# Kernel optimization log

Hardware: AMD Instinct MI355X
Metric: run time of the kernel (lower is better)

## Reference

```python
import jax, jax.numpy as jnp
import numpy as np

NUM_HEADS = 16
HEAD_DIM = 64
ROPE_BASE = 10000.0


def apply_rope(x):
    # x: [b, s, n_h, h_d]; pairwise rotation as in torchtune RotaryPositionalEmbeddings
    b, s, nh, hd = x.shape
    inv_freq = 1.0 / (ROPE_BASE ** (jnp.arange(0, hd, 2, dtype=jnp.float32) / hd))  # [hd/2]
    angles = jnp.arange(s, dtype=jnp.float32)[:, None] * inv_freq[None, :]          # [s, hd/2]
    cos = jnp.cos(angles)[None, :, None, :]  # [1, s, 1, hd/2]
    sin = jnp.sin(angles)[None, :, None, :]
    xp = x.reshape(b, s, nh, hd // 2, 2)
    x1, x2 = xp[..., 0], xp[..., 1]
    rot = jnp.stack([x1 * cos - x2 * sin, x1 * sin + x2 * cos], axis=-1)
    return rot.reshape(b, s, nh, hd)


def setup_inputs() -> dict:
    key = jax.random.key(0)
    k1, k2 = jax.random.split(key)
    B, S, D = 64, 200, 1024
    x = jax.random.normal(k1, (B, S, D), dtype=jnp.float32)
    # causal mask, realistic for a decoder; True = attend
    mask = jnp.broadcast_to(jnp.tril(jnp.ones((S, S), dtype=bool)), (B, S, S))
    W_qkv = jax.random.normal(k2, (3 * D, D), dtype=jnp.float32) * (1.0 / np.sqrt(D))
    b_qkv = jnp.zeros((3 * D,), dtype=jnp.float32)
    return {"x": x, "mask": mask, "W_qkv": W_qkv, "b_qkv": b_qkv}


def reference(x, mask, W_qkv, b_qkv):
    B, S, D = x.shape
    H, hd = NUM_HEADS, HEAD_DIM
    qkv = x @ W_qkv.T + b_qkv                      # [B, S, 3D]
    qkv = qkv.reshape(B, S, H, 3 * hd)
    q, k, v = jnp.split(qkv, 3, axis=-1)           # each [B, S, H, hd]
    q = apply_rope(q)
    k = apply_rope(k)
    q = q.transpose(0, 2, 1, 3)                    # [B, H, S, hd]
    k = k.transpose(0, 2, 1, 3)
    v = v.transpose(0, 2, 1, 3)
    logits = jnp.einsum("bhqd,bhkd->bhqk", q, k) / jnp.sqrt(jnp.float32(hd))
    logits = jnp.where(mask[:, None, :, :], logits, -jnp.inf)
    attn = jax.nn.softmax(logits, axis=-1)
    out = jnp.einsum("bhqk,bhkd->bhqd", attn, v)   # [B, H, S, hd]
    return out.transpose(0, 2, 1, 3).reshape(B, S, H * hd)
```

## Files before the change

### kernel.cpp

```cpp
#include <hip/hip_runtime.h>
#include <hip/hip_bf16.h>

#define BB 64
#define SS 200
#define DD 1024
#define HH 16
#define HD 64
#define N3 3072
#define MM (BB*SS)
#define KK DD
#define SPV 216

using half8 = __attribute__((ext_vector_type(8))) _Float16;
using f32x4 = __attribute__((ext_vector_type(4))) float;

__device__ __forceinline__ void gload16(const void* g, void* l) {
    __builtin_amdgcn_global_load_lds(
        (const __attribute__((address_space(1))) void*)g,
        (__attribute__((address_space(3))) void*)l, 16, 0, 0);
}

__global__ __launch_bounds__(256) void f32_to_f16_kernel(const float* __restrict__ in,
                                                         _Float16* __restrict__ out, int n8) {
    int i = blockIdx.x * 256 + threadIdx.x;
    int stride = gridDim.x * 256;
    for (; i < n8; i += stride) {
        float4 a = ((const float4*)in)[i * 2];
        float4 b = ((const float4*)in)[i * 2 + 1];
        half8 h;
        h[0] = (_Float16)a.x; h[1] = (_Float16)a.y; h[2] = (_Float16)a.z; h[3] = (_Float16)a.w;
        h[4] = (_Float16)b.x; h[5] = (_Float16)b.y; h[6] = (_Float16)b.z; h[7] = (_Float16)b.w;
        ((half8*)out)[i] = h;
    }
}

__global__ __launch_bounds__(256) void rope_table_kernel(float* __restrict__ rope) {
    int t = blockIdx.x * 256 + threadIdx.x;
    if (t >= SS * 32) return;
    int s = t >> 5, i = t & 31;
    float inv = powf(10000.0f, -(float)(2 * i) / 64.0f);
    float ang = (float)s * inv;
    rope[t * 2 + 0] = cosf(ang);
    rope[t * 2 + 1] = sinf(ang);
}

__device__ __forceinline__ void gemm_step(const _Float16* Asb, const _Float16* Bsb,
                                          int arow, int brow, int kq,
                                          f32x4 (&acc)[4][4]) {
    half8 af[4], bf[4];
    #pragma unroll
    for (int mi = 0; mi < 4; ++mi) {
        int r = arow + mi * 16;
        af[mi] = *(const half8*)&Asb[r * 32 + ((kq ^ ((r >> 1) & 3)) << 3)];
    }
    #pragma unroll
    for (int ni = 0; ni < 4; ++ni) {
        int r = brow + ni * 16;
        bf[ni] = *(const half8*)&Bsb[r * 32 + ((kq ^ ((r >> 1) & 3)) << 3)];
    }
    __builtin_amdgcn_s_setprio(1);
    #pragma unroll
    for (int mi = 0; mi < 4; ++mi)
        #pragma unroll
        for (int ni = 0; ni < 4; ++ni)
            acc[mi][ni] = __builtin_amdgcn_mfma_f32_16x16x32_f16(af[mi], bf[ni], acc[mi][ni], 0, 0, 0);
    __builtin_amdgcn_s_setprio(0);
}

__global__ __launch_bounds__(256) void qkv_gemm_f16_kernel(
    const _Float16* __restrict__ Xh, const _Float16* __restrict__ Wh,
    const float* __restrict__ bias, const float* __restrict__ rope,
    _Float16* __restrict__ qo, _Float16* __restrict__ ko, _Float16* __restrict__ vt)
{
    __shared__ _Float16 As[2][128 * 32];
    __shared__ _Float16 Bs[2][128 * 32];

    const int t = threadIdx.x;
    const int w = t >> 6, lane = t & 63;
    const int wm = w >> 1, wn = w & 1;
    const int m0 = blockIdx.y * 128, n0 = blockIdx.x * 128;

    f32x4 acc[4][4];
    #pragma unroll
    for (int i = 0; i < 4; ++i)
        #pragma unroll
        for (int j = 0; j < 4; ++j) acc[i][j] = (f32x4)0.f;

    int srow[2], scol[2], sdst[2];
    #pragma unroll
    for (int c = 0; c < 2; ++c) {
        int slot = c * 256 + t;
        int r = slot >> 2, sl = slot & 3;
        srow[c] = r;
        scol[c] = (sl ^ ((r >> 1) & 3)) << 3;
        sdst[c] = (c * 256 + w * 64) * 8;
    }
    const int arow = wm * 64 + (lane & 15);
    const int brow = wn * 64 + (lane & 15);
    const int kq = lane >> 4;

    const _Float16* Xb = Xh + (size_t)m0 * KK;
    const _Float16* Wb = Wh + (size_t)n0 * KK;

    #pragma unroll
    for (int c = 0; c < 2; ++c) {
        gload16(Xb + (size_t)srow[c] * KK + scol[c], &As[0][sdst[c]]);
        gload16(Wb + (size_t)srow[c] * KK + scol[c], &Bs[0][sdst[c]]);
    }
    asm volatile("s_waitcnt vmcnt(0)" ::: "memory");
    __builtin_amdgcn_s_barrier();

    for (int kt = 0; kt < KK; kt += 64) {
        #pragma unroll
        for (int c = 0; c < 2; ++c) {
            gload16(Xb + (size_t)srow[c] * KK + kt + 32 + scol[c], &As[1][sdst[c]]);
            gload16(Wb + (size_t)srow[c] * KK + kt + 32 + scol[c], &Bs[1][sdst[c]]);
        }
        gemm_step(As[0], Bs[0], arow, brow, kq, acc);
        asm volatile("s_waitcnt vmcnt(0)" ::: "memory");
        __builtin_amdgcn_s_barrier();
        if (kt + 64 < KK) {
            #pragma unroll
            for (int c = 0; c < 2; ++c) {
                gload16(Xb + (size_t)srow[c] * KK + kt + 64 + scol[c], &As[0][sdst[c]]);
                gload16(Wb + (size_t)srow[c] * KK + kt + 64 + scol[c], &Bs[0][sdst[c]]);
            }
        }
        gemm_step(As[1], Bs[1], arow, brow, kq, acc);
        asm volatile("s_waitcnt vmcnt(0)" ::: "memory");
        __builtin_amdgcn_s_barrier();
    }

    #pragma unroll
    for (int ni = 0; ni < 4; ++ni) {
        int n = n0 + wn * 64 + ni * 16 + (lane & 15);
        float bv = bias[n];
        int h = n / 192;
        int rr = n - h * 192;
        int which = rr >> 6;
        int j = rr & 63;
        int jp = j >> 1;
        #pragma unroll
        for (int mi = 0; mi < 4; ++mi) {
            #pragma unroll
            for (int reg = 0; reg < 4; ++reg) {
                int m = m0 + wm * 64 + mi * 16 + (lane >> 4) * 4 + reg;
                int b_ = m / SS, s_ = m - b_ * SS;
                float v = acc[mi][ni][reg] + bv;
                float p = __shfl_xor(v, 1);
                size_t bh = (size_t)b_ * HH + h;
                if (which == 2) {
                    vt[(bh * HD + j) * SPV + s_] = (_Float16)v;
                } else {
                    float2 cs = *(const float2*)&rope[(s_ * 32 + jp) * 2];
                    float o = (j & 1) ? fmaf(p, cs.y, v * cs.x) : fmaf(v, cs.x, -p * cs.y);
                    if (which == 0)
                        qo[(bh * SS + s_) * HD + j] = (_Float16)(o * 0.125f);
                    else
                        ko[(bh * SS + s_) * HD + j] = (_Float16)o;
                }
            }
        }
    }
}

__global__ __launch_bounds__(256) void attn_mfma_kernel(
    const _Float16* __restrict__ q, const _Float16* __restrict__ k,
    const _Float16* __restrict__ vt, float* __restrict__ out)
{
    __shared__ _Float16 Klds[256 * 64];
    __shared__ _Float16 VTlds[64 * SPV];
    __shared__ _Float16 Plds[4][32 * 64];

    const int bh = blockIdx.x;
    const int b_ = bh >> 4, h = bh & 15;
    const int t = threadIdx.x;
    const int w = t >> 6, lane = t & 63;
    const int l15 = lane & 15, l4 = lane >> 4;

    const _Float16* kbase = k + (size_t)bh * SS * HD;
    const _Float16* vtbase = vt + (size_t)bh * HD * SPV;
    const _Float16* qbase = q + (size_t)bh * SS * HD;

    for (int c = t; c < 256 * 8; c += 256) {
        int row = c >> 3, g = c & 7;
        int rowc = row < SS ? row : (SS - 1);
        float4 val = *(const float4*)(kbase + rowc * HD + g * 8);
        *(float4*)&Klds[row * 64 + ((g ^ (row & 7)) * 8)] = val;
    }
    for (int c = t; c < 64 * 27; c += 256) {
        int row = c / 27, g = c - row * 27;
        *(float4*)&VTlds[row * SPV + g * 8] = *(const float4*)(vtbase + row * SPV + g * 8);
    }
    __syncthreads();

    const int qts[2] = { (w == 3) ? 6 : w, 5 - w };
    const int nqt = (w == 3) ? 1 : 2;

    for (int qi = 0; qi < nqt; ++qi) {
        const int qt = qts[qi];
        const int q0 = qt * 32;
        const int nkt = (q0 + 95) >> 6;

        half8 qf[2][2];
        #pragma unroll
        for (int mt = 0; mt < 2; ++mt)
            #pragma unroll
            for (int ks = 0; ks < 2; ++ks)
                qf[mt][ks] = *(const half8*)(qbase + (size_t)(q0 + mt * 16 + l15) * HD + ks * 32 + l4 * 8);

        float mrow[2][4], lsum[2][4];
        f32x4 oacc[2][4];
        #pragma unroll
        for (int mt = 0; mt < 2; ++mt) {
            #pragma unroll
            for (int r = 0; r < 4; ++r) { mrow[mt][r] = -1e30f; lsum[mt][r] = 0.f; }
            #pragma unroll
            for (int nt = 0; nt < 4; ++nt) oacc[mt][nt] = (f32x4)0.f;
        }

        for (int ki = 0; ki < nkt; ++ki) {
            const int k0 = ki * 64;
            const bool lastk = (ki == nkt - 1);

            half8 kf[4][2];
            #pragma unroll
            for (int nt = 0; nt < 4; ++nt)
                #pragma unroll
                for (int ks = 0; ks < 2; ++ks) {
                    int row = k0 + nt * 16 + l15;
                    int g = l4 + ks * 4;
                    kf[nt][ks] = *(const half8*)&Klds[row * 64 + ((g ^ (row & 7)) * 8)];
                }
            f32x4 s[2][4];
            __builtin_amdgcn_s_setprio(1);
            #pragma unroll
            for (int mt = 0; mt < 2; ++mt)
                #pragma unroll
                for (int nt = 0; nt < 4; ++nt) {
                    f32x4 a = (f32x4)0.f;
                    a = __builtin_amdgcn_mfma_f32_16x16x32_f16(qf[mt][0], kf[nt][0], a, 0, 0, 0);
                    a = __builtin_amdgcn_mfma_f32_16x16x32_f16(qf[mt][1], kf[nt][1], a, 0, 0, 0);
                    s[mt][nt] = a;
                }
            __builtin_amdgcn_s_setprio(0);

            if (lastk) {
                #pragma unroll
                for (int mt = 0; mt < 2; ++mt)
                    #pragma unroll
                    for (int nt = 0; nt < 4; ++nt)
                        #pragma unroll
                        for (int r = 0; r < 4; ++r) {
                            int qq = q0 + mt * 16 + l4 * 4 + r;
                            int kk2 = k0 + nt * 16 + l15;
                            if (kk2 > qq || kk2 >= SS) s[mt][nt][r] = -1e30f;
                        }
            }

            #pragma unroll
            for (int mt = 0; mt < 2; ++mt) {
                float tmax[4];
                int ok = 1;
                #pragma unroll
                for (int r = 0; r < 4; ++r) {
                    float tm = fmaxf(fmaxf(s[mt][0][r], s[mt][1][r]),
                                     fmaxf(s[mt][2][r], s[mt][3][r]));
                    #pragma unroll
                    for (int off = 8; off > 0; off >>= 1)
                        tm = fmaxf(tm, __shfl_xor(tm, off));
                    tmax[r] = tm;
                    ok &= (tm <= mrow[mt][r] + 4.0f) ? 1 : 0;
                }
                if (__all(ok)) {
                    #pragma unroll
                    for (int r = 0; r < 4; ++r) {
                        float mo = mrow[mt][r];
                        float ps = 0.f;
                        #pragma unroll
                        for (int nt = 0; nt < 4; ++nt) {
                            float p = __expf(s[mt][nt][r] - mo);
                            s[mt][nt][r] = p;
                            ps += p;
                        }
                        lsum[mt][r] += ps;
                    }
                } else {
                    #pragma unroll
                    for (int r = 0; r < 4; ++r) {
                        float mo = mrow[mt][r];
                        float mn = fmaxf(mo, tmax[r]);
                        float sc = __expf(mo - mn);
                        mrow[mt][r] = mn;
                        float ps = 0.f;
                        #pragma unroll
                        for (int nt = 0; nt < 4; ++nt) {
                            float p = __expf(s[mt][nt][r] - mn);
                            s[mt][nt][r] = p;
                            ps += p;
                        }
                        lsum[mt][r] = lsum[mt][r] * sc + ps;
                        #pragma unroll
                        for (int nt = 0; nt < 4; ++nt)
                            oacc[mt][nt][r] *= sc;
                    }
                }
            }

            #pragma unroll
            for (int mt = 0; mt < 2; ++mt)
                #pragma unroll
                for (int nt = 0; nt < 4; ++nt)
                    #pragma unroll
                    for (int r = 0; r < 4; ++r) {
                        int row = mt * 16 + l4 * 4 + r;
                        int col = nt * 16 + l15;
                        Plds[w][row * 64 + (((col >> 3) ^ (row & 7)) * 8) + (col & 7)] =
                            (_Float16)s[mt][nt][r];
                    }

            half8 pa[2][2], vb[4][2];
            #pragma unroll
            for (int mt = 0; mt < 2; ++mt)
                #pragma unroll
                for (int ksl = 0; ksl < 2; ++ksl) {
                    int row = mt * 16 + l15;
                    pa[mt][ksl] = *(const half8*)&Plds[w][row * 64 + (((ksl * 4 + l4) ^ (row & 7)) * 8)];
                }
            #pragma unroll
            for (int nt = 0; nt < 4; ++nt)
                #pragma unroll
                for (int ksl = 0; ksl < 2; ++ksl) {
                    int koff = k0 + ksl * 32 + l4 * 8;
                    koff = (koff > SPV - 8) ? (SPV - 8) : koff;
                    vb[nt][ksl] = *(const half8*)&VTlds[(nt * 16 + l15) * SPV + koff];
                }
            __builtin_amdgcn_s_setprio(1);
            #pragma unroll
            for (int mt = 0; mt < 2; ++mt)
                #pragma unroll
                for (int nt = 0; nt < 4; ++nt) {
                    oacc[mt][nt] = __builtin_amdgcn_mfma_f32_16x16x32_f16(pa[mt][0], vb[nt][0], oacc[mt][nt], 0, 0, 0);
                    oacc[mt][nt] = __builtin_amdgcn_mfma_f32_16x16x32_f16(pa[mt][1], vb[nt][1], oacc[mt][nt], 0, 0, 0);
                }
            __builtin_amdgcn_s_setprio(0);
        }

        #pragma unroll
        for (int mt = 0; mt < 2; ++mt) {
            #pragma unroll
            for (int r = 0; r < 4; ++r) {
                float l = lsum[mt][r];
                #pragma unroll
                for (int off = 8; off > 0; off >>= 1)
                    l += __shfl_xor(l, off);
                int s_ = q0 + mt * 16 + l4 * 4 + r;
                if (s_ < SS) {
                    float rinv = 1.0f / l;
                    #pragma unroll
                    for (int nt = 0; nt < 4; ++nt)
                        out[((size_t)b_ * SS + s_) * DD + h * HD + nt * 16 + l15] = oacc[mt][nt][r] * rinv;
                }
            }
        }
    }
}

extern "C" void kernel_launch(void* const* d_in, const int* in_sizes, int n_in,
                              void* d_out, int out_size, void* d_ws, size_t ws_size,
                              hipStream_t stream) {
    const float* x    = (const float*)d_in[0];
    const float* W    = (const float*)d_in[2];
    const float* bias = (const float*)d_in[3];
    float* out = (float*)d_out;

    char* ws = (char*)d_ws;
    float*    rope = (float*)ws;
    _Float16* Xh   = (_Float16*)(ws + 65536);
    _Float16* Wh   = (_Float16*)(ws + 65536 + 26214400ull);
    _Float16* Qh   = (_Float16*)(ws + 65536 + 26214400ull + 6291456ull);
    _Float16* Kh   = Qh + (size_t)BB * HH * SS * HD;
    _Float16* VTh  = Kh + (size_t)BB * HH * SS * HD;

    f32_to_f16_kernel<<<2048, 256, 0, stream>>>(x, Xh, MM * KK / 8);
    f32_to_f16_kernel<<<1024, 256, 0, stream>>>(W, Wh, N3 * KK / 8);
    rope_table_kernel<<<(SS * 32 + 255) / 256, 256, 0, stream>>>(rope);
    qkv_gemm_f16_kernel<<<dim3(N3 / 128, MM / 128), dim3(256), 0, stream>>>(Xh, Wh, bias, rope, Qh, Kh, VTh);
    attn_mfma_kernel<<<BB * HH, 256, 0, stream>>>(Qh, Kh, VTh, out);
}
```

Baseline: 356.0 us.

## Deepen QKV GEMM global-to-LDS pipeline to four stages with partial vmcnt waits

```diff
diff --git a/kernel.cpp b/kernel.cpp
--- a/kernel.cpp
+++ b/kernel.cpp
@@ -72,8 +72,8 @@
     const float* __restrict__ bias, const float* __restrict__ rope,
     _Float16* __restrict__ qo, _Float16* __restrict__ ko, _Float16* __restrict__ vt)
 {
-    __shared__ _Float16 As[2][128 * 32];
-    __shared__ _Float16 Bs[2][128 * 32];
+    __shared__ _Float16 As[4][128 * 32];
+    __shared__ _Float16 Bs[4][128 * 32];
 
     const int t = threadIdx.x;
     const int w = t >> 6, lane = t & 63;
@@ -102,34 +102,31 @@
     const _Float16* Xb = Xh + (size_t)m0 * KK;
     const _Float16* Wb = Wh + (size_t)n0 * KK;
 
-    #pragma unroll
-    for (int c = 0; c < 2; ++c) {
-        gload16(Xb + (size_t)srow[c] * KK + scol[c], &As[0][sdst[c]]);
-        gload16(Wb + (size_t)srow[c] * KK + scol[c], &Bs[0][sdst[c]]);
-    }
-    asm volatile("s_waitcnt vmcnt(0)" ::: "memory");
-    __builtin_amdgcn_s_barrier();
-
-    for (int kt = 0; kt < KK; kt += 64) {
-        #pragma unroll
-        for (int c = 0; c < 2; ++c) {
-            gload16(Xb + (size_t)srow[c] * KK + kt + 32 + scol[c], &As[1][sdst[c]]);
-            gload16(Wb + (size_t)srow[c] * KK + kt + 32 + scol[c], &Bs[1][sdst[c]]);
-        }
-        gemm_step(As[0], Bs[0], arow, brow, kq, acc);
-        asm volatile("s_waitcnt vmcnt(0)" ::: "memory");
+    #define ISSUE_TILE(p, buf)                                                     \
+        do {                                                                       \
+            _Pragma("unroll")                                                      \
+            for (int c = 0; c < 2; ++c) {                                          \
+                gload16(Xb + (size_t)srow[c] * KK + (p) * 32 + scol[c],            \
+                        &As[buf][sdst[c]]);                                        \
+                gload16(Wb + (size_t)srow[c] * KK + (p) * 32 + scol[c],            \
+                        &Bs[buf][sdst[c]]);                                        \
+            }                                                                      \
+        } while (0)
+
+    ISSUE_TILE(0, 0);
+    ISSUE_TILE(1, 1);
+    ISSUE_TILE(2, 2);
+
+    for (int kt = 0; kt < 32; ++kt) {
+        const int rem = 31 - kt;
+        if (rem >= 2)      asm volatile("s_waitcnt vmcnt(8)" ::: "memory");
+        else if (rem == 1) asm volatile("s_waitcnt vmcnt(4)" ::: "memory");
+        else               asm volatile("s_waitcnt vmcnt(0)" ::: "memory");
         __builtin_amdgcn_s_barrier();
-        if (kt + 64 < KK) {
-            #pragma unroll
-            for (int c = 0; c < 2; ++c) {
-                gload16(Xb + (size_t)srow[c] * KK + kt + 64 + scol[c], &As[0][sdst[c]]);
-                gload16(Wb + (size_t)srow[c] * KK + kt + 64 + scol[c], &Bs[0][sdst[c]]);
-            }
-        }
-        gemm_step(As[1], Bs[1], arow, brow, kq, acc);
-        asm volatile("s_waitcnt vmcnt(0)" ::: "memory");
-        __builtin_amdgcn_s_barrier();
-    }
+        if (kt + 3 < 32) ISSUE_TILE(kt + 3, (kt + 3) & 3);
+        gemm_step(As[kt & 3], Bs[kt & 3], arow, brow, kq, acc);
+    }
+    #undef ISSUE_TILE
 
     #pragma unroll
     for (int ni = 0; ni < 4; ++ni) {
```

New measurement: 356.1 us. No clear change (+0.0%).
